# Kernel optimization log

Hardware: AMD Instinct MI355X
Metric: run time of the kernel (lower is better)

## Reference

```python
import jax, jax.numpy as jnp
import numpy as np

EMB = 768
NH = 12
DH = EMB // NH
NORM = float(np.sqrt(DH))  # 8.0


def setup_inputs() -> dict:
    key = jax.random.key(0)
    ks = jax.random.split(key, 9)
    B, S = 1, 4096
    s = 0.02  # realistic init scale for weights
    return {
        "x": jax.random.normal(ks[0], (B, S, EMB), jnp.float32),
        "mask": jnp.ones((B, S), jnp.float32),
        "Wq": jax.random.normal(ks[1], (EMB, EMB), jnp.float32) * s,
        "bq": jnp.zeros((EMB,), jnp.float32),
        "Wk": jax.random.normal(ks[2], (EMB, EMB), jnp.float32) * s,
        "bk": jnp.zeros((EMB,), jnp.float32),
        "Wv": jax.random.normal(ks[3], (EMB, EMB), jnp.float32) * s,
        "bv": jnp.zeros((EMB,), jnp.float32),
        "Wo": jax.random.normal(ks[4], (EMB, EMB), jnp.float32) * s,
        "bo": jnp.zeros((EMB,), jnp.float32),
    }


def reference(x, mask, Wq, bq, Wk, bk, Wv, bv, Wo, bo):
    B, S, _ = x.shape
    # QKV projections (torch Linear: x @ W.T + b)
    q = x @ Wq.T + bq
    k = x @ Wk.T + bk
    v = x @ Wv.T + bv
    # split heads: b s (nh dh) -> b nh s dh
    split = lambda t: t.reshape(B, S, NH, DH).transpose(0, 2, 1, 3)
    qh, kh, vh = split(q), split(k), split(v)
    # attention scores [b, nh, s, s]
    scores = jnp.einsum("bhqd,bhkd->bhqk", qh, kh) / NORM
    # additive mask: scores -= 10000 * (1 - mask), mask broadcast over query dim
    scores = scores - 10000.0 * (1.0 - mask[:, None, None, :])
    attn = jax.nn.softmax(scores, axis=-1)
    out = jnp.einsum("bhqk,bhkd->bhqd", attn, vh)
    # b nh s dh -> b s (nh dh)
    out = out.transpose(0, 2, 1, 3).reshape(B, S, EMB)
    return out @ Wo.T + bo
```

## Files before the change

kernel.cpp:

```cpp
#include <hip/hip_runtime.h>
#include <stdint.h>
#include <stddef.h>

#define EMB 768
#define SEQ 4096
#define NH 12
#define DH 64
#define LOG2E 1.44269504f
#define NSP 2
#define SPLEN (SEQ / NSP)
#define NBLK (NH * 32 * NSP)

typedef __attribute__((ext_vector_type(8))) short short8;
typedef __attribute__((ext_vector_type(4))) float f32x4;
typedef __attribute__((ext_vector_type(16))) float f32x16;
typedef __attribute__((ext_vector_type(2))) unsigned int uint32x2;

static __device__ __forceinline__ unsigned short f2bf(float f) {
  union { float f; uint32_t u; } v; v.f = f;
  uint32_t u = v.u;
  return (unsigned short)((u + 0x7FFFu + ((u >> 16) & 1u)) >> 16);
}
static __device__ __forceinline__ float bf2f(unsigned short s) {
  union { uint32_t u; float f; } v; v.u = ((uint32_t)s) << 16;
  return v.f;
}

static __device__ __forceinline__ void gl_lds16(const void* g, void* l) {
  __builtin_amdgcn_global_load_lds(
      (const __attribute__((address_space(1))) uint32_t*)g,
      (__attribute__((address_space(3))) uint32_t*)l, 16, 0, 0);
}
static __device__ __forceinline__ void gl_lds4(const void* g, void* l) {
  __builtin_amdgcn_global_load_lds(
      (const __attribute__((address_space(1))) uint32_t*)g,
      (__attribute__((address_space(3))) uint32_t*)l, 4, 0, 0);
}

__global__ void prep_kernel(const float* __restrict__ x, const float* __restrict__ mask,
                            const float* __restrict__ Wq, const float* __restrict__ Wk,
                            const float* __restrict__ Wv, const float* __restrict__ Wo,
                            unsigned short* __restrict__ xb, unsigned short* __restrict__ wqb,
                            unsigned short* __restrict__ wkb, unsigned short* __restrict__ wvb,
                            unsigned short* __restrict__ wob, float* __restrict__ mb2) {
  const int y = blockIdx.y;
  if (y == 5) {
    int i = blockIdx.x * 256 + threadIdx.x;
    if (i < SEQ) mb2[i] = -80000.f * (1.f - mask[i]);
    return;
  }
  const float* in = y == 0 ? x : y == 1 ? Wq : y == 2 ? Wk : y == 3 ? Wv : Wo;
  unsigned short* out = y == 0 ? xb : y == 1 ? wqb : y == 2 ? wkb : y == 3 ? wvb : wob;
  const int n = (y == 0) ? SEQ * EMB : EMB * EMB;
  int stride = gridDim.x * blockDim.x * 4;
  for (int i = (blockIdx.x * blockDim.x + threadIdx.x) * 4; i < n; i += stride) {
    float4 v = *reinterpret_cast<const float4*>(in + i);
    ushort4 o;
    o.x = f2bf(v.x); o.y = f2bf(v.y); o.z = f2bf(v.z); o.w = f2bf(v.w);
    *reinterpret_cast<ushort4*>(out + i) = o;
  }
}

__global__ void norm1_kernel(const unsigned short* __restrict__ Qb,
                             const unsigned short* __restrict__ Kb,
                             float* __restrict__ pbnd) {
  const int mh = blockIdx.x;
  const int mat = mh / NH;
  const int head = mh % NH;
  const unsigned short* base = (mat == 0 ? Qb : Kb) + head * DH;
  const int t = threadIdx.x;
  const int slot = t & 7;
  const int rloc = t >> 3;
  float mx = 0.f;
#pragma unroll
  for (int p = 0; p < 4; ++p) {
    int row = blockIdx.y * 128 + p * 32 + rloc;
    short8 v = *reinterpret_cast<const short8*>(base + (size_t)row * EMB + slot * 8);
    float s = 0.f;
#pragma unroll
    for (int j = 0; j < 8; ++j) {
      float f = bf2f((unsigned short)v[j]);
      s = fmaf(f, f, s);
    }
#pragma unroll
    for (int off = 1; off < 8; off <<= 1)
      s += __shfl_xor(s, off, 64);
    mx = fmaxf(mx, s);
  }
#pragma unroll
  for (int off = 8; off < 64; off <<= 1)
    mx = fmaxf(mx, __shfl_xor(mx, off, 64));
  __shared__ float wmax[4];
  if ((t & 63) == 0) wmax[t >> 6] = mx;
  __syncthreads();
  if (t == 0)
    pbnd[mh * 32 + blockIdx.y] =
        fmaxf(fmaxf(wmax[0], wmax[1]), fmaxf(wmax[2], wmax[3]));
}

__global__ void norm2_kernel(const float* __restrict__ pbnd,
                             unsigned int* __restrict__ bnd) {
  int i = threadIdx.x;
  if (i < 2 * NH) {
    float m = 0.f;
#pragma unroll
    for (int c = 0; c < 32; ++c) m = fmaxf(m, pbnd[i * 32 + c]);
    bnd[i] = __float_as_uint(sqrtf(m));
  }
}

template <int OUT_F32>
static __device__ __forceinline__ void gemm64(
    const unsigned short* __restrict__ A, const unsigned short* __restrict__ W,
    const float* __restrict__ bias, void* __restrict__ Cout,
    int M, int N, int K, int bm, int bn) {
  __shared__ unsigned short Alds[64 * 64];
  __shared__ unsigned short Blds[128 * 64];
  const int t = threadIdx.x;
  const int lane = t & 63;
  const int wave = t >> 6;
  const int wr = wave >> 1, wc = wave & 1;
  const int lm = lane & 15, lg = lane >> 4;

  f32x4 acc[2][4];
#pragma unroll
  for (int i = 0; i < 2; ++i)
#pragma unroll
    for (int j = 0; j < 4; ++j) acc[i][j] = (f32x4){0.f, 0.f, 0.f, 0.f};

  const int srow = t >> 3;
  const int scsw = (t & 7) * 16;

  const int nK = K >> 6;
  for (int kt = 0; kt < nK; ++kt) {
    const int k0 = kt << 6;
#pragma unroll
    for (int i = 0; i < 2; ++i) {
      int row = i * 32 + srow;
      int cb = scsw ^ ((row & 7) << 4);
      gl_lds16(A + (size_t)(bm * 64 + row) * K + k0 + (cb >> 1),
               (char*)Alds + i * 4096 + t * 16);
    }
#pragma unroll
    for (int i = 0; i < 4; ++i) {
      int row = i * 32 + srow;
      int cb = scsw ^ ((row & 7) << 4);
      gl_lds16(W + (size_t)(bn * 128 + row) * K + k0 + (cb >> 1),
               (char*)Blds + i * 4096 + t * 16);
    }
    __syncthreads();
#pragma unroll
    for (int kk = 0; kk < 2; ++kk) {
      short8 af[2], bfr[4];
#pragma unroll
      for (int i = 0; i < 2; ++i) {
        int rowa = wr * 32 + i * 16 + lm;
        int cba = (kk * 64 + lg * 16) ^ ((rowa & 7) << 4);
        af[i] = *reinterpret_cast<const short8*>((const char*)Alds + rowa * 128 + cba);
      }
#pragma unroll
      for (int j = 0; j < 4; ++j) {
        int rowb = wc * 64 + j * 16 + lm;
        int cbb = (kk * 64 + lg * 16) ^ ((rowb & 7) << 4);
        bfr[j] = *reinterpret_cast<const short8*>((const char*)Blds + rowb * 128 + cbb);
      }
#pragma unroll
      for (int i = 0; i < 2; ++i)
#pragma unroll
        for (int j = 0; j < 4; ++j)
          acc[i][j] = __builtin_amdgcn_mfma_f32_16x16x32_bf16(af[i], bfr[j], acc[i][j], 0, 0, 0);
    }
    __syncthreads();
  }
#pragma unroll
  for (int i = 0; i < 2; ++i) {
    int row0 = bm * 64 + wr * 32 + i * 16 + lg * 4;
#pragma unroll
    for (int j = 0; j < 4; ++j) {
      int col = bn * 128 + wc * 64 + j * 16 + lm;
      float b = bias[col];
#pragma unroll
      for (int r = 0; r < 4; ++r) {
        float v = acc[i][j][r] + b;
        if (OUT_F32)
          ((float*)Cout)[(size_t)(row0 + r) * N + col] = v;
        else
          ((unsigned short*)Cout)[(size_t)(row0 + r) * N + col] = f2bf(v);
      }
    }
  }
}

__global__ __launch_bounds__(256, 2) void gemm_wo(
    const unsigned short* __restrict__ A, const unsigned short* __restrict__ W,
    const float* __restrict__ bias, float* __restrict__ C) {
  gemm64<1>(A, W, bias, C, SEQ, EMB, EMB, blockIdx.x, blockIdx.y);
}

__global__ __launch_bounds__(256, 2) void qkv_gemm(
    const unsigned short* __restrict__ A,
    const unsigned short* __restrict__ W0, const unsigned short* __restrict__ W1,
    const unsigned short* __restrict__ W2,
    const float* __restrict__ b0, const float* __restrict__ b1, const float* __restrict__ b2,
    unsigned short* __restrict__ O0, unsigned short* __restrict__ O1,
    unsigned short* __restrict__ O2) {
  const int z = blockIdx.z;
  const unsigned short* W = z == 0 ? W0 : z == 1 ? W1 : W2;
  const float* bias = z == 0 ? b0 : z == 1 ? b1 : b2;
  unsigned short* O = z == 0 ? O0 : z == 1 ? O1 : O2;
  gemm64<0>(A, W, bias, O, SEQ, EMB, EMB, blockIdx.x, blockIdx.y);
}

__global__ void transpose_kernel(const unsigned short* __restrict__ in,
                                 unsigned short* __restrict__ out) {
  __shared__ unsigned short tile[32][33];
  int tx = threadIdx.x, ty = threadIdx.y;
  int e0 = blockIdx.x * 32, s0 = blockIdx.y * 32;
#pragma unroll
  for (int i = 0; i < 4; ++i)
    tile[ty + i * 8][tx] = in[(size_t)(s0 + ty + i * 8) * EMB + e0 + tx];
  __syncthreads();
#pragma unroll
  for (int i = 0; i < 4; ++i)
    out[(size_t)(e0 + ty + i * 8) * SEQ + s0 + tx] = tile[tx][ty + i * 8];
}

__global__ __launch_bounds__(256, 3) void attn_kernel(
    const unsigned short* __restrict__ Q, const unsigned short* __restrict__ Kb,
    const unsigned short* __restrict__ Vt, const float* __restrict__ mb2,
    const unsigned int* __restrict__ bnd,
    unsigned short* __restrict__ opart, float* __restrict__ lpart) {
  __shared__ unsigned short Klds[2][64 * DH];
  __shared__ unsigned short Vlds[2][DH * 64];
  __shared__ __align__(16) float msk[2][64];

  const int t = threadIdx.x;
  const int lane = t & 63;
  const int wave = t >> 6;
  const int o = blockIdx.x;
  const int wg = (o & 7) * (NBLK / 8) + (o >> 3);
  const int head = wg >> 6;
  const int rem = wg & 63;
  const int qb = rem >> 1;
  const int sp = rem & 1;
  const int q0 = qb * 128 + wave * 32;
  const int kvb0 = sp * SPLEN;
  const int lm = lane & 31;
  const int h = lane >> 5;

  const float sc2 = 0.125f * LOG2E;
  union { unsigned int u; float f; } qn, kn;
  qn.u = bnd[head]; kn.u = bnd[NH + head];
  const float mfix = qn.f * kn.f * sc2;

  short8 qf[4];
#pragma unroll
  for (int ks = 0; ks < 4; ++ks)
    qf[ks] = *reinterpret_cast<const short8*>(
        Q + (size_t)(q0 + lm) * EMB + head * DH + ks * 16 + h * 8);

  short8 ones;
#pragma unroll
  for (int i = 0; i < 8; ++i) ones[i] = (short)0x3F80;

  f32x16 oacc[2], lacc;
#pragma unroll
  for (int n = 0; n < 2; ++n)
#pragma unroll
    for (int r = 0; r < 16; ++r) oacc[n][r] = 0.f;
#pragma unroll
  for (int r = 0; r < 16; ++r) lacc[r] = 0.f;

  const int srow = t >> 3;
  const int scol = (t & 7) * 16;

  auto STAGE = [&](int buf, int kt2) {
    const int kv0 = kvb0 + kt2 * 64;
#pragma unroll
    for (int i = 0; i < 2; ++i) {
      int row = i * 32 + srow;
      int cb = scol ^ ((row & 7) << 4);
      gl_lds16(Kb + (size_t)(kv0 + row) * EMB + head * DH + (cb >> 1),
               (char*)Klds + buf * 8192 + i * 4096 + t * 16);
      gl_lds16(Vt + (size_t)(head * DH + row) * SEQ + kv0 + (cb >> 1),
               (char*)Vlds + buf * 8192 + i * 4096 + t * 16);
    }
    gl_lds4(mb2 + kv0 + lane, &msk[buf][0]);
  };

  constexpr int NT = SPLEN / 64;
  STAGE(0, 0);
  __syncthreads();

  for (int kt = 0; kt < NT; ++kt) {
    const int buf = kt & 1;
    if (kt + 1 < NT) STAGE(buf ^ 1, kt + 1);

    f32x16 s[2];
#pragma unroll
    for (int tt = 0; tt < 2; ++tt)
#pragma unroll
      for (int a = 0; a < 4; ++a) {
        f32x4 m = *reinterpret_cast<const f32x4*>(&msk[buf][tt * 32 + a * 8 + h * 4]);
#pragma unroll
        for (int i = 0; i < 4; ++i) s[tt][a * 4 + i] = m[i];
      }

    __builtin_amdgcn_s_setprio(1);
#pragma unroll
    for (int tt = 0; tt < 2; ++tt)
#pragma unroll
      for (int ks = 0; ks < 4; ++ks) {
        int row = tt * 32 + lm;
        int cb = (ks * 32 + h * 16) ^ ((row & 7) << 4);
        short8 kf = *reinterpret_cast<const short8*>(
            (const char*)Klds + buf * 8192 + row * 128 + cb);
        s[tt] = __builtin_amdgcn_mfma_f32_32x32x16_bf16(kf, qf[ks], s[tt], 0, 0, 0);
      }
    __builtin_amdgcn_s_setprio(0);

#pragma unroll
    for (int tt = 0; tt < 2; ++tt)
#pragma unroll
      for (int r = 0; r < 16; ++r)
        s[tt][r] = __builtin_amdgcn_exp2f(fmaf(s[tt][r], sc2, -mfix));

    short8 pa[4];
#pragma unroll
    for (int tt = 0; tt < 2; ++tt) {
      uint32_t r0[4], r1[4];
#pragma unroll
      for (int a = 0; a < 4; ++a) {
        asm("v_cvt_pk_bf16_f32 %0, %1, %2" : "=v"(r0[a]) : "v"(s[tt][4 * a]), "v"(s[tt][4 * a + 1]));
        asm("v_cvt_pk_bf16_f32 %0, %1, %2" : "=v"(r1[a]) : "v"(s[tt][4 * a + 2]), "v"(s[tt][4 * a + 3]));
      }
#pragma unroll
      for (int ksl = 0; ksl < 2; ++ksl) {
        uint32x2 w0 = __builtin_amdgcn_permlane32_swap(r0[2 * ksl], r0[2 * ksl + 1], false, false);
        uint32x2 w1 = __builtin_amdgcn_permlane32_swap(r1[2 * ksl], r1[2 * ksl + 1], false, false);
        union { short8 s8; uint32_t u[4]; } pk;
        pk.u[0] = w0[0]; pk.u[1] = w1[0]; pk.u[2] = w0[1]; pk.u[3] = w1[1];
        pa[tt * 2 + ksl] = pk.s8;
      }
    }

    __builtin_amdgcn_s_setprio(1);
#pragma unroll
    for (int n = 0; n < 2; ++n)
#pragma unroll
      for (int ks = 0; ks < 4; ++ks) {
        int row = n * 32 + lm;
        int cb = (ks * 32 + h * 16) ^ ((row & 7) << 4);
        short8 vf = *reinterpret_cast<const short8*>(
            (const char*)Vlds + buf * 8192 + row * 128 + cb);
        oacc[n] = __builtin_amdgcn_mfma_f32_32x32x16_bf16(pa[ks], vf, oacc[n], 0, 0, 0);
      }
#pragma unroll
    for (int ks = 0; ks < 4; ++ks)
      lacc = __builtin_amdgcn_mfma_f32_32x32x16_bf16(pa[ks], ones, lacc, 0, 0, 0);
    __builtin_amdgcn_s_setprio(0);

    __syncthreads();
  }

  f32x16 rl;
#pragma unroll
  for (int r = 0; r < 16; ++r) rl[r] = __builtin_amdgcn_rcpf(lacc[r]);
  unsigned short* ob = opart + ((size_t)(sp * NH + head) * SEQ + q0) * 64;
#pragma unroll
  for (int n = 0; n < 2; ++n)
#pragma unroll
    for (int r = 0; r < 16; ++r) {
      int crow = (r & 3) + 8 * (r >> 2) + 4 * h;
      ob[crow * 64 + n * 32 + lm] = f2bf(oacc[n][r] * rl[r]);
    }
  const size_t pbase = (size_t)(sp * NH + head) * SEQ + q0;
  if (lm == 0) {
#pragma unroll
    for (int r = 0; r < 16; ++r) {
      int crow = (r & 3) + 8 * (r >> 2) + 4 * h;
      lpart[pbase + crow] = lacc[r];
    }
  }
}

__global__ void merge_kernel(const unsigned short* __restrict__ opart,
                             const float* __restrict__ lpart,
                             unsigned short* __restrict__ Ab) {
  int tid = blockIdx.x * 256 + threadIdx.x;
  int dv = tid & 15;
  int rq = tid >> 4;
  int head = rq >> 12;
  int q = rq & 4095;
  size_t base = (size_t)head * SEQ + q;
  const size_t str = (size_t)NH * SEQ;

  float l0 = lpart[base], l1 = lpart[base + str];
  float rd = 1.0f / (l0 + l1);
  float c0 = l0 * rd, c1 = l1 * rd;

  ushort4 o0 = *reinterpret_cast<const ushort4*>(opart + base * 64 + dv * 4);
  ushort4 o1 = *reinterpret_cast<const ushort4*>(opart + (base + str) * 64 + dv * 4);
  ushort4 r;
  r.x = f2bf(c0 * bf2f(o0.x) + c1 * bf2f(o1.x));
  r.y = f2bf(c0 * bf2f(o0.y) + c1 * bf2f(o1.y));
  r.z = f2bf(c0 * bf2f(o0.z) + c1 * bf2f(o1.z));
  r.w = f2bf(c0 * bf2f(o0.w) + c1 * bf2f(o1.w));
  *reinterpret_cast<ushort4*>(Ab + (size_t)q * EMB + head * DH + dv * 4) = r;
}

extern "C" void kernel_launch(void* const* d_in, const int* in_sizes, int n_in,
                              void* d_out, int out_size, void* d_ws, size_t ws_size,
                              hipStream_t stream) {
  const float* x    = (const float*)d_in[0];
  const float* mask = (const float*)d_in[1];
  const float* Wq   = (const float*)d_in[2];
  const float* bq   = (const float*)d_in[3];
  const float* Wk   = (const float*)d_in[4];
  const float* bk   = (const float*)d_in[5];
  const float* Wv   = (const float*)d_in[6];
  const float* bv   = (const float*)d_in[7];
  const float* Wo   = (const float*)d_in[8];
  const float* bo   = (const float*)d_in[9];
  float* out = (float*)d_out;

  char* ws = (char*)d_ws;
  const size_t SZ_X = (size_t)SEQ * EMB * 2;
  const size_t SZ_W = (size_t)EMB * EMB * 2;
  unsigned short* xb  = (unsigned short*)(ws);
  unsigned short* wqb = (unsigned short*)(ws + SZ_X);
  unsigned short* wkb = (unsigned short*)(ws + SZ_X + SZ_W);
  unsigned short* wvb = (unsigned short*)(ws + SZ_X + 2 * SZ_W);
  unsigned short* wob = (unsigned short*)(ws + SZ_X + 3 * SZ_W);
  unsigned short* Qb  = (unsigned short*)(ws + SZ_X + 4 * SZ_W);
  unsigned short* Kbuf= (unsigned short*)(ws + 2 * SZ_X + 4 * SZ_W);
  unsigned short* Vb  = (unsigned short*)(ws + 3 * SZ_X + 4 * SZ_W);
  unsigned short* Vtb = (unsigned short*)(ws + 4 * SZ_X + 4 * SZ_W);
  unsigned short* Ab  = (unsigned short*)(ws + 5 * SZ_X + 4 * SZ_W);
  size_t off = 6 * SZ_X + 4 * SZ_W;
  float* mb2            = (float*)(ws + off);          off += (size_t)SEQ * 4;
  unsigned short* opart = (unsigned short*)(ws + off); off += (size_t)NSP * NH * SEQ * 64 * 2;
  float* lpart          = (float*)(ws + off);          off += (size_t)NSP * NH * SEQ * 4;
  unsigned int* bnd     = (unsigned int*)(ws + off);   off += 256;
  float* pbnd           = (float*)(ws + off);

  prep_kernel<<<dim3(192, 6), 256, 0, stream>>>(
      x, mask, Wq, Wk, Wv, Wo, xb, wqb, wkb, wvb, wob, mb2);

  qkv_gemm<<<dim3(SEQ / 64, EMB / 128, 3), 256, 0, stream>>>(
      xb, wqb, wkb, wvb, bq, bk, bv, Qb, Kbuf, Vb);

  norm1_kernel<<<dim3(2 * NH, 32), 256, 0, stream>>>(Qb, Kbuf, pbnd);
  norm2_kernel<<<1, 64, 0, stream>>>(pbnd, bnd);

  transpose_kernel<<<dim3(EMB / 32, SEQ / 32), dim3(32, 8), 0, stream>>>(Vb, Vtb);

  attn_kernel<<<NBLK, 256, 0, stream>>>(Qb, Kbuf, Vtb, mb2, bnd, opart, lpart);
  merge_kernel<<<3072, 256, 0, stream>>>(opart, lpart, Ab);

  gemm_wo<<<dim3(SEQ / 64, EMB / 128), 256, 0, stream>>>(Ab, wob, bo, out);
}
```

Measured before the change: 129.6 us.

## Fuse split-KV merge into output projection GEMM A-tile loading

Removes the merge kernel and the intermediate attention-output buffer. A small kernel now computes per-row combine weights from the two split partial sums, and the Wo GEMM loads both partial outputs, blends them in registers and writes the result into shared memory as its A tile. This drops a full write and read of the merged activations. In exchange, every column block of the GEMM redoes the blend and reads two partial tiles, and the A loads become synchronous register loads instead of direct-to-LDS copies.

```diff
diff --git a/kernel.cpp b/kernel.cpp
--- a/kernel.cpp
+++ b/kernel.cpp
@@ -107,6 +107,12 @@
     for (int c = 0; c < 32; ++c) m = fmaxf(m, pbnd[i * 32 + c]);
     bnd[i] = __float_as_uint(sqrtf(m));
   }
+}
+
+__global__ void lw_kernel(const float* __restrict__ lpart, float* __restrict__ cbuf) {
+  int i = blockIdx.x * 256 + threadIdx.x;
+  float l0 = lpart[i], l1 = lpart[i + NH * SEQ];
+  cbuf[i] = l0 / (l0 + l1);
 }
 
 template <int OUT_F32>
@@ -191,12 +197,6 @@
   }
 }
 
-__global__ __launch_bounds__(256, 2) void gemm_wo(
-    const unsigned short* __restrict__ A, const unsigned short* __restrict__ W,
-    const float* __restrict__ bias, float* __restrict__ C) {
-  gemm64<1>(A, W, bias, C, SEQ, EMB, EMB, blockIdx.x, blockIdx.y);
-}
-
 __global__ __launch_bounds__(256, 2) void qkv_gemm(
     const unsigned short* __restrict__ A,
     const unsigned short* __restrict__ W0, const unsigned short* __restrict__ W1,
@@ -209,6 +209,94 @@
   const float* bias = z == 0 ? b0 : z == 1 ? b1 : b2;
   unsigned short* O = z == 0 ? O0 : z == 1 ? O1 : O2;
   gemm64<0>(A, W, bias, O, SEQ, EMB, EMB, blockIdx.x, blockIdx.y);
+}
+
+__global__ __launch_bounds__(256, 2) void gemm_wo_fused(
+    const unsigned short* __restrict__ opart, const float* __restrict__ cbuf,
+    const unsigned short* __restrict__ W, const float* __restrict__ bias,
+    float* __restrict__ C) {
+  __shared__ unsigned short Alds[64 * 64];
+  __shared__ unsigned short Blds[128 * 64];
+  const int t = threadIdx.x;
+  const int lane = t & 63;
+  const int wave = t >> 6;
+  const int wr = wave >> 1, wc = wave & 1;
+  const int lm = lane & 15, lg = lane >> 4;
+  const int bm = blockIdx.x, bn = blockIdx.y;
+
+  f32x4 acc[2][4];
+#pragma unroll
+  for (int i = 0; i < 2; ++i)
+#pragma unroll
+    for (int j = 0; j < 4; ++j) acc[i][j] = (f32x4){0.f, 0.f, 0.f, 0.f};
+
+  const int srow = t >> 3;
+  const int scsw = (t & 7) * 16;
+
+  const int nK = EMB >> 6;
+  for (int kt = 0; kt < nK; ++kt) {
+    const int k0 = kt << 6;
+#pragma unroll
+    for (int i = 0; i < 2; ++i) {
+      int row = i * 32 + srow;
+      int q = bm * 64 + row;
+      int cb = scsw ^ ((row & 7) << 4);
+      int d = cb >> 1;
+      float c0 = cbuf[kt * SEQ + q];
+      float c1 = 1.f - c0;
+      size_t ob = ((size_t)kt * SEQ + q) * 64 + d;
+      short8 o0 = *reinterpret_cast<const short8*>(opart + ob);
+      short8 o1 = *reinterpret_cast<const short8*>(opart + (size_t)NH * SEQ * 64 + ob);
+      short8 m;
+#pragma unroll
+      for (int e = 0; e < 8; ++e)
+        m[e] = (short)f2bf(c0 * bf2f((unsigned short)o0[e]) +
+                           c1 * bf2f((unsigned short)o1[e]));
+      *reinterpret_cast<short8*>((char*)Alds + i * 4096 + t * 16) = m;
+    }
+#pragma unroll
+    for (int i = 0; i < 4; ++i) {
+      int row = i * 32 + srow;
+      int cb = scsw ^ ((row & 7) << 4);
+      gl_lds16(W + (size_t)(bn * 128 + row) * EMB + k0 + (cb >> 1),
+               (char*)Blds + i * 4096 + t * 16);
+    }
+    __syncthreads();
+#pragma unroll
+    for (int kk = 0; kk < 2; ++kk) {
+      short8 af[2], bfr[4];
+#pragma unroll
+      for (int i = 0; i < 2; ++i) {
+        int rowa = wr * 32 + i * 16 + lm;
+        int cba = (kk * 64 + lg * 16) ^ ((rowa & 7) << 4);
+        af[i] = *reinterpret_cast<const short8*>((const char*)Alds + rowa * 128 + cba);
+      }
+#pragma unroll
+      for (int j = 0; j < 4; ++j) {
+        int rowb = wc * 64 + j * 16 + lm;
+        int cbb = (kk * 64 + lg * 16) ^ ((rowb & 7) << 4);
+        bfr[j] = *reinterpret_cast<const short8*>((const char*)Blds + rowb * 128 + cbb);
+      }
+#pragma unroll
+      for (int i = 0; i < 2; ++i)
+#pragma unroll
+        for (int j = 0; j < 4; ++j)
+          acc[i][j] = __builtin_amdgcn_mfma_f32_16x16x32_bf16(af[i], bfr[j], acc[i][j], 0, 0, 0);
+    }
+    __syncthreads();
+  }
+#pragma unroll
+  for (int i = 0; i < 2; ++i) {
+    int row0 = bm * 64 + wr * 32 + i * 16 + lg * 4;
+#pragma unroll
+    for (int j = 0; j < 4; ++j) {
+      int col = bn * 128 + wc * 64 + j * 16 + lm;
+      float b = bias[col];
+#pragma unroll
+      for (int r = 0; r < 4; ++r)
+        C[(size_t)(row0 + r) * EMB + col] = acc[i][j][r] + b;
+    }
+  }
 }
 
 __global__ void transpose_kernel(const unsigned short* __restrict__ in,
@@ -382,31 +470,6 @@
       lpart[pbase + crow] = lacc[r];
     }
   }
-}
-
-__global__ void merge_kernel(const unsigned short* __restrict__ opart,
-                             const float* __restrict__ lpart,
-                             unsigned short* __restrict__ Ab) {
-  int tid = blockIdx.x * 256 + threadIdx.x;
-  int dv = tid & 15;
-  int rq = tid >> 4;
-  int head = rq >> 12;
-  int q = rq & 4095;
-  size_t base = (size_t)head * SEQ + q;
-  const size_t str = (size_t)NH * SEQ;
-
-  float l0 = lpart[base], l1 = lpart[base + str];
-  float rd = 1.0f / (l0 + l1);
-  float c0 = l0 * rd, c1 = l1 * rd;
-
-  ushort4 o0 = *reinterpret_cast<const ushort4*>(opart + base * 64 + dv * 4);
-  ushort4 o1 = *reinterpret_cast<const ushort4*>(opart + (base + str) * 64 + dv * 4);
-  ushort4 r;
-  r.x = f2bf(c0 * bf2f(o0.x) + c1 * bf2f(o1.x));
-  r.y = f2bf(c0 * bf2f(o0.y) + c1 * bf2f(o1.y));
-  r.z = f2bf(c0 * bf2f(o0.z) + c1 * bf2f(o1.z));
-  r.w = f2bf(c0 * bf2f(o0.w) + c1 * bf2f(o1.w));
-  *reinterpret_cast<ushort4*>(Ab + (size_t)q * EMB + head * DH + dv * 4) = r;
 }
 
 extern "C" void kernel_launch(void* const* d_in, const int* in_sizes, int n_in,
@@ -436,13 +499,13 @@
   unsigned short* Kbuf= (unsigned short*)(ws + 2 * SZ_X + 4 * SZ_W);
   unsigned short* Vb  = (unsigned short*)(ws + 3 * SZ_X + 4 * SZ_W);
   unsigned short* Vtb = (unsigned short*)(ws + 4 * SZ_X + 4 * SZ_W);
-  unsigned short* Ab  = (unsigned short*)(ws + 5 * SZ_X + 4 * SZ_W);
-  size_t off = 6 * SZ_X + 4 * SZ_W;
+  size_t off = 5 * SZ_X + 4 * SZ_W;
   float* mb2            = (float*)(ws + off);          off += (size_t)SEQ * 4;
   unsigned short* opart = (unsigned short*)(ws + off); off += (size_t)NSP * NH * SEQ * 64 * 2;
   float* lpart          = (float*)(ws + off);          off += (size_t)NSP * NH * SEQ * 4;
   unsigned int* bnd     = (unsigned int*)(ws + off);   off += 256;
-  float* pbnd           = (float*)(ws + off);
+  float* pbnd           = (float*)(ws + off);          off += 1024;
+  float* cbuf           = (float*)(ws + off);
 
   prep_kernel<<<dim3(192, 6), 256, 0, stream>>>(
       x, mask, Wq, Wk, Wv, Wo, xb, wqb, wkb, wvb, wob, mb2);
@@ -456,7 +519,9 @@
   transpose_kernel<<<dim3(EMB / 32, SEQ / 32), dim3(32, 8), 0, stream>>>(Vb, Vtb);
 
   attn_kernel<<<NBLK, 256, 0, stream>>>(Qb, Kbuf, Vtb, mb2, bnd, opart, lpart);
-  merge_kernel<<<3072, 256, 0, stream>>>(opart, lpart, Ab);
-
-  gemm_wo<<<dim3(SEQ / 64, EMB / 128), 256, 0, stream>>>(Ab, wob, bo, out);
-}
+
+  lw_kernel<<<NH * SEQ / 256, 256, 0, stream>>>(lpart, cbuf);
+
+  gemm_wo_fused<<<dim3(SEQ / 64, EMB / 128), 256, 0, stream>>>(
+      opart, cbuf, wob, bo, out);
+}
```

Result: slower. 134.0 us (+3.5%).
